# Performance work log

Measured on AMD Instinct MI355X. Metric: run time of the kernel, lower is better.

The kernel has to match this reference:

```python
import jax, jax.numpy as jnp
import numpy as np

N_NODES = 50000
N_EDGES = 800000
NFEAT, NHID, NCLASS = 512, 256, 128
N_UV = 2048


def gcn_layer(x, adj_row, adj_col, adj_val, W, b):
    # support = x @ W ; out = A @ support (sparse COO spmm) + b
    support = x @ W                                   # [N, out]
    msgs = adj_val[:, None] * support[adj_col]        # [E, out]
    out = jax.ops.segment_sum(msgs, adj_row, num_segments=N_NODES)
    return out + b


def setup_inputs() -> dict:
    key = jax.random.key(0)
    ks = jax.random.split(key, 12)
    u = jax.random.randint(ks[0], (N_UV,), 0, N_NODES)
    v = jax.random.randint(ks[1], (N_UV,), 0, N_NODES)
    x = jax.random.normal(ks[2], (N_NODES, NFEAT), dtype=jnp.float32)
    adj_row = jnp.sort(jax.random.randint(ks[3], (N_EDGES,), 0, N_NODES))
    adj_col = jax.random.randint(ks[4], (N_EDGES,), 0, N_NODES)
    adj_val = jax.random.uniform(ks[5], (N_EDGES,), dtype=jnp.float32)
    s1 = 1.0 / np.sqrt(NHID)
    s2 = 1.0 / np.sqrt(NCLASS)
    W1 = jax.random.uniform(ks[6], (NFEAT, NHID), minval=-s1, maxval=s1, dtype=jnp.float32)
    b1 = jax.random.uniform(ks[7], (NHID,), minval=-s1, maxval=s1, dtype=jnp.float32)
    W2 = jax.random.uniform(ks[8], (NHID, NCLASS), minval=-s2, maxval=s2, dtype=jnp.float32)
    b2 = jax.random.uniform(ks[9], (NCLASS,), minval=-s2, maxval=s2, dtype=jnp.float32)
    We = jax.random.normal(ks[10], (NCLASS, NCLASS), dtype=jnp.float32) * (1.0 / np.sqrt(NCLASS))
    return {"u": u, "v": v, "x": x, "adj_row": adj_row, "adj_col": adj_col,
            "adj_val": adj_val, "W1": W1, "b1": b1, "W2": W2, "b2": b2, "We": We}


def reference(u, v, x, adj_row, adj_col, adj_val, W1, b1, W2, b2, We):
    # layer 1: GCN + ReLU (dropout is identity in eval mode)
    h = jax.nn.relu(gcn_layer(x, adj_row, adj_col, adj_val, W1, b1))
    # layer 2: GCN
    z = gcn_layer(h, adj_row, adj_col, adj_val, W2, b2)          # [N, nclass]
    # edge scoring: sigmoid(w_edge(z[u]) @ z[v].T)
    zu = z[u] @ We.T                                             # [U, nclass] (nn.Linear: x @ W.T)
    zv = z[v]                                                    # [V, nclass]
    p_uv = jax.nn.sigmoid(zu @ zv.T)                             # [U, V]
    return p_uv
```

## Files before the change

### kernel.cpp

```cpp
#include <hip/hip_runtime.h>
#include <hip/hip_bf16.h>
#include <math.h>

#define N_NODES 50000
#define N_EDGES 800000
#define NFEAT   512
#define NHID    256
#define NCLASS  128
#define N_UV    2048

#define Q24_SCALE  524288.0f
#define Q24_INV    1.9073486328125e-6f

typedef __bf16    bf16x8 __attribute__((ext_vector_type(8)));
typedef short     s16x8  __attribute__((ext_vector_type(8)));
typedef float     f32x4  __attribute__((ext_vector_type(4)));

struct __attribute__((packed)) U3 { unsigned a, b, c; };

__device__ __forceinline__ unsigned short bf16_rn(float f) {
  unsigned u = __float_as_uint(f);
  u += 0x7fffu + ((u >> 16) & 1u);
  return (unsigned short)(u >> 16);
}
__device__ __forceinline__ float bf16_to_f(unsigned short h) {
  return __uint_as_float(((unsigned)h) << 16);
}
__device__ __forceinline__ void unpack24(unsigned a, unsigned b, unsigned c,
                                         int& e0, int& e1, int& e2, int& e3) {
  e0 = ((int)(a << 8)) >> 8;
  e1 = ((int)((b << 16) | ((a >> 24) << 8))) >> 8;
  e2 = ((int)((c << 24) | ((b >> 16) << 8))) >> 8;
  e3 = ((int)c) >> 8;
}

#define LDSPAD 72

template <bool ASPLIT, bool BSPLIT, int OMODE>
__global__ __launch_bounds__(256, 2) void gemm_mfma_split(
    const float* __restrict__ Af,
    const unsigned short* __restrict__ Ahi, const unsigned short* __restrict__ Alo,
    const float* __restrict__ BTf,
    const unsigned short* __restrict__ BThi, const unsigned short* __restrict__ BTlo,
    float* __restrict__ C, unsigned char* __restrict__ Cq, int M, int N, int K) {
  __shared__ unsigned short sAh[128 * LDSPAD];
  __shared__ unsigned short sAl[128 * LDSPAD];
  __shared__ unsigned short sBh[128 * LDSPAD];
  __shared__ unsigned short sBl[128 * LDSPAD];

  const int tid  = threadIdx.x;
  const int lane = tid & 63;
  const int wave = tid >> 6;
  const int wm   = (wave >> 1) << 6;
  const int wn   = (wave & 1) << 6;
  const int lm   = lane & 15;
  const int quad = lane >> 4;
  const int m0   = blockIdx.y * 128;
  const int n0   = blockIdx.x * 128;

  const int r32 = tid >> 4;
  const int c32 = (tid & 15) * 4;
  const int r16 = tid >> 3;
  const int c16 = (tid & 7) * 8;

  float4 pA[8]; s16x8 pAh[4], pAl[4];
  float4 pB[8]; s16x8 pBh[4], pBl[4];

  f32x4 acc[4][4];
#pragma unroll
  for (int i = 0; i < 4; ++i)
#pragma unroll
    for (int j = 0; j < 4; ++j)
#pragma unroll
      for (int r = 0; r < 4; ++r) acc[i][j][r] = 0.f;

#define LOAD_TILE(k0)                                                          \
  do {                                                                         \
    if (ASPLIT) {                                                              \
      _Pragma("unroll") for (int p = 0; p < 8; ++p) {                          \
        const int m = m0 + p * 16 + r32;                                       \
        pA[p] = make_float4(0.f, 0.f, 0.f, 0.f);                               \
        if (m < M) pA[p] = *(const float4*)&Af[(size_t)m * K + (k0) + c32];    \
      }                                                                        \
    } else {                                                                   \
      _Pragma("unroll") for (int p = 0; p < 4; ++p) {                          \
        const int m = m0 + p * 32 + r16;                                       \
        _Pragma("unroll") for (int e = 0; e < 8; ++e) { pAh[p][e] = 0; pAl[p][e] = 0; } \
        if (m < M) {                                                           \
          pAh[p] = *(const s16x8*)&Ahi[(size_t)m * K + (k0) + c16];            \
          pAl[p] = *(const s16x8*)&Alo[(size_t)m * K + (k0) + c16];            \
        }                                                                      \
      }                                                                        \
    }                                                                          \
    if (BSPLIT) {                                                              \
      _Pragma("unroll") for (int p = 0; p < 8; ++p) {                          \
        const int n = n0 + p * 16 + r32;                                       \
        pB[p] = *(const float4*)&BTf[(size_t)n * K + (k0) + c32];              \
      }                                                                        \
    } else {                                                                   \
      _Pragma("unroll") for (int p = 0; p < 4; ++p) {                          \
        pBh[p] = *(const s16x8*)&BThi[(size_t)(n0 + p * 32 + r16) * K + (k0) + c16]; \
        pBl[p] = *(const s16x8*)&BTlo[(size_t)(n0 + p * 32 + r16) * K + (k0) + c16]; \
      }                                                                        \
    }                                                                          \
  } while (0)

#define SPLIT4(v, hv, lv)                                                      \
  hv.x = bf16_rn(v.x); lv.x = bf16_rn(v.x - bf16_to_f(hv.x));                  \
  hv.y = bf16_rn(v.y); lv.y = bf16_rn(v.y - bf16_to_f(hv.y));                  \
  hv.z = bf16_rn(v.z); lv.z = bf16_rn(v.z - bf16_to_f(hv.z));                  \
  hv.w = bf16_rn(v.w); lv.w = bf16_rn(v.w - bf16_to_f(hv.w));

#define STORE_TILE()                                                           \
  do {                                                                         \
    if (ASPLIT) {                                                              \
      _Pragma("unroll") for (int p = 0; p < 8; ++p) {                          \
        ushort4 hv, lv; SPLIT4(pA[p], hv, lv);                                 \
        const int row = p * 16 + r32;                                          \
        *(ushort4*)&sAh[row * LDSPAD + c32] = hv;                              \
        *(ushort4*)&sAl[row * LDSPAD + c32] = lv;                              \
      }                                                                        \
    } else {                                                                   \
      _Pragma("unroll") for (int p = 0; p < 4; ++p) {                          \
        const int row = p * 32 + r16;                                          \
        *(s16x8*)&sAh[row * LDSPAD + c16] = pAh[p];                            \
        *(s16x8*)&sAl[row * LDSPAD + c16] = pAl[p];                            \
      }                                                                        \
    }                                                                          \
    if (BSPLIT) {                                                              \
      _Pragma("unroll") for (int p = 0; p < 8; ++p) {                          \
        ushort4 hv, lv; SPLIT4(pB[p], hv, lv);                                 \
        const int row = p * 16 + r32;                                          \
        *(ushort4*)&sBh[row * LDSPAD + c32] = hv;                              \
        *(ushort4*)&sBl[row * LDSPAD + c32] = lv;                              \
      }                                                                        \
    } else {                                                                   \
      _Pragma("unroll") for (int p = 0; p < 4; ++p) {                          \
        const int row = p * 32 + r16;                                          \
        *(s16x8*)&sBh[row * LDSPAD + c16] = pBh[p];                            \
        *(s16x8*)&sBl[row * LDSPAD + c16] = pBl[p];                            \
      }                                                                        \
    }                                                                          \
  } while (0)

  LOAD_TILE(0);

  for (int k0 = 0; k0 < K; k0 += 64) {
    if (k0) __syncthreads();
    STORE_TILE();
    __syncthreads();
    if (k0 + 64 < K) LOAD_TILE(k0 + 64);

#pragma unroll
    for (int ks = 0; ks < 2; ++ks) {
      const int koff = ks * 32 + quad * 8;
      bf16x8 aH[4], aL[4], bH[4], bL[4];
#pragma unroll
      for (int i = 0; i < 4; ++i) {
        const int r = wm + i * 16 + lm;
        aH[i] = __builtin_bit_cast(bf16x8, *(const s16x8*)&sAh[r * LDSPAD + koff]);
        aL[i] = __builtin_bit_cast(bf16x8, *(const s16x8*)&sAl[r * LDSPAD + koff]);
      }
#pragma unroll
      for (int j = 0; j < 4; ++j) {
        const int r = wn + j * 16 + lm;
        bH[j] = __builtin_bit_cast(bf16x8, *(const s16x8*)&sBh[r * LDSPAD + koff]);
        bL[j] = __builtin_bit_cast(bf16x8, *(const s16x8*)&sBl[r * LDSPAD + koff]);
      }
#pragma unroll
      for (int i = 0; i < 4; ++i)
#pragma unroll
        for (int j = 0; j < 4; ++j) {
          acc[i][j] = __builtin_amdgcn_mfma_f32_16x16x32_bf16(aH[i], bH[j], acc[i][j], 0, 0, 0);
          acc[i][j] = __builtin_amdgcn_mfma_f32_16x16x32_bf16(aH[i], bL[j], acc[i][j], 0, 0, 0);
          acc[i][j] = __builtin_amdgcn_mfma_f32_16x16x32_bf16(aL[i], bH[j], acc[i][j], 0, 0, 0);
        }
    }
  }

#pragma unroll
  for (int i = 0; i < 4; ++i)
#pragma unroll
    for (int j = 0; j < 4; ++j) {
      const int col = n0 + wn + j * 16 + lm;
#pragma unroll
      for (int r = 0; r < 4; ++r) {
        const int row = m0 + wm + i * 16 + quad * 4 + r;
        if (row < M) {
          float v = acc[i][j][r];
          if (OMODE == 1) {
            v = 1.f / (1.f + expf(-v));
            C[(size_t)row * N + col] = v;
          } else if (OMODE == 2) {
            int q = __float2int_rn(v * Q24_SCALE);
            q = q > 8388607 ? 8388607 : (q < -8388608 ? -8388608 : q);
            unsigned char* p = Cq + ((size_t)row * N + col) * 3;
            p[0] = (unsigned char)(q & 0xFF);
            p[1] = (unsigned char)((q >> 8) & 0xFF);
            p[2] = (unsigned char)((q >> 16) & 0xFF);
          } else {
            C[(size_t)row * N + col] = v;
          }
        }
      }
    }
#undef LOAD_TILE
#undef STORE_TILE
#undef SPLIT4
}

__global__ __launch_bounds__(256) void prep_all(
    const int* __restrict__ rows, int* __restrict__ row_ptr,
    const float* __restrict__ W1, unsigned short* __restrict__ W1Thi,
    unsigned short* __restrict__ W1Tlo,
    const float* __restrict__ W2, unsigned short* __restrict__ W2Thi,
    unsigned short* __restrict__ W2Tlo) {
  const int idx = blockIdx.x * 256 + threadIdx.x;
  if (idx < N_EDGES) {
    const int r = rows[idx];
    const int rprev = (idx == 0) ? -1 : rows[idx - 1];
    for (int n = rprev + 1; n <= r; ++n) row_ptr[n] = idx;
    if (idx == N_EDGES - 1)
      for (int n = r + 1; n <= N_NODES; ++n) row_ptr[n] = N_EDGES;
  }
  if (idx < NFEAT * NHID) {
    const int n = idx / NFEAT;
    const int k = idx - n * NFEAT;
    const float f = W1[(size_t)k * NHID + n];
    const unsigned short h = bf16_rn(f);
    W1Thi[idx] = h;
    W1Tlo[idx] = bf16_rn(f - bf16_to_f(h));
  }
  if (idx < NHID * NCLASS) {
    const int n = idx / NHID;
    const int k = idx - n * NHID;
    const float f = W2[(size_t)k * NCLASS + n];
    const unsigned short h = bf16_rn(f);
    W2Thi[idx] = h;
    W2Tlo[idx] = bf16_rn(f - bf16_to_f(h));
  }
}

__global__ __launch_bounds__(256, 4) void spmm256_q24_split(
    const unsigned char* __restrict__ Sq, const int* __restrict__ row_ptr,
    const int* __restrict__ cols, const float* __restrict__ vals,
    const float4* __restrict__ bias4,
    unsigned short* __restrict__ outHi, unsigned short* __restrict__ outLo) {
  const int wave = threadIdx.x >> 6;
  const int lane = threadIdx.x & 63;
  const int node = blockIdx.x * 4 + wave;

  const int lou = __builtin_amdgcn_readfirstlane(row_ptr[node]);
  const int hiu = __builtin_amdgcn_readfirstlane(row_ptr[node + 1]);

  float4 acc = make_float4(0.f, 0.f, 0.f, 0.f);
  const int lane12 = lane * 12;

  for (int base = lou; base < hiu; base += 16) {
    int   c[16];
    float w[16];
    if (base + 16 <= hiu) {
#pragma unroll
      for (int t = 0; t < 16; ++t) {
        c[t] = cols[base + t];
        w[t] = vals[base + t] * Q24_INV;
      }
    } else {
#pragma unroll
      for (int t = 0; t < 16; ++t) {
        const int idx = base + t;
        const int ide = idx < hiu ? idx : hiu - 1;
        c[t] = cols[ide];
        w[t] = idx < hiu ? vals[ide] * Q24_INV : 0.f;
      }
    }
    U3 d[16];
#pragma unroll
    for (int t = 0; t < 16; ++t)
      d[t] = *(const U3*)&Sq[(size_t)c[t] * (NHID * 3) + lane12];
#pragma unroll
    for (int t = 0; t < 16; ++t) {
      int e0, e1, e2, e3;
      unpack24(d[t].a, d[t].b, d[t].c, e0, e1, e2, e3);
      acc.x = fmaf(w[t], (float)e0, acc.x);
      acc.y = fmaf(w[t], (float)e1, acc.y);
      acc.z = fmaf(w[t], (float)e2, acc.z);
      acc.w = fmaf(w[t], (float)e3, acc.w);
    }
  }

  const float4 b = bias4[lane];
  acc.x = fmaxf(acc.x + b.x, 0.f);
  acc.y = fmaxf(acc.y + b.y, 0.f);
  acc.z = fmaxf(acc.z + b.z, 0.f);
  acc.w = fmaxf(acc.w + b.w, 0.f);

  ushort4 hv, lv;
  hv.x = bf16_rn(acc.x); lv.x = bf16_rn(acc.x - bf16_to_f(hv.x));
  hv.y = bf16_rn(acc.y); lv.y = bf16_rn(acc.y - bf16_to_f(hv.y));
  hv.z = bf16_rn(acc.z); lv.z = bf16_rn(acc.z - bf16_to_f(hv.z));
  hv.w = bf16_rn(acc.w); lv.w = bf16_rn(acc.w - bf16_to_f(hv.w));
  const size_t o = (size_t)node * NHID + lane * 4;
  *(ushort4*)&outHi[o] = hv;
  *(ushort4*)&outLo[o] = lv;
}

__global__ __launch_bounds__(256) void spmm128_f32_list(
    const float4* __restrict__ S4, const int* __restrict__ row_ptr,
    const int* __restrict__ cols, const float* __restrict__ vals,
    const float4* __restrict__ bias4,
    const int* __restrict__ u, const int* __restrict__ v,
    float4* __restrict__ out4) {
  const int wave = threadIdx.x >> 6;
  const int lane = threadIdx.x & 63;
  const int half = lane >> 5;
  const int l32  = lane & 31;
  const int idx  = blockIdx.x * 4 + wave;
  const int node = idx < N_UV ? u[idx] : v[idx - N_UV];

  const int lo = row_ptr[node];
  const int hi = row_ptr[node + 1];

  float4 acc = make_float4(0.f, 0.f, 0.f, 0.f);
  int e = lo + half;
  for (; e + 6 < hi; e += 8) {
    int c[4]; float w[4];
#pragma unroll
    for (int t = 0; t < 4; ++t) { c[t] = cols[e + 2 * t]; w[t] = vals[e + 2 * t]; }
    float4 r[4];
#pragma unroll
    for (int t = 0; t < 4; ++t) r[t] = S4[(size_t)c[t] * 32 + l32];
#pragma unroll
    for (int t = 0; t < 4; ++t) {
      acc.x = fmaf(w[t], r[t].x, acc.x); acc.y = fmaf(w[t], r[t].y, acc.y);
      acc.z = fmaf(w[t], r[t].z, acc.z); acc.w = fmaf(w[t], r[t].w, acc.w);
    }
  }
  for (; e < hi; e += 2) {
    const int c = cols[e];
    const float w = vals[e];
    const float4 r = S4[(size_t)c * 32 + l32];
    acc.x = fmaf(w, r.x, acc.x); acc.y = fmaf(w, r.y, acc.y);
    acc.z = fmaf(w, r.z, acc.z); acc.w = fmaf(w, r.w, acc.w);
  }

  acc.x += __shfl_xor(acc.x, 32);
  acc.y += __shfl_xor(acc.y, 32);
  acc.z += __shfl_xor(acc.z, 32);
  acc.w += __shfl_xor(acc.w, 32);

  if (half == 0) {
    const float4 b = bias4[l32];
    acc.x += b.x; acc.y += b.y; acc.z += b.z; acc.w += b.w;
    out4[(size_t)idx * 32 + l32] = acc;
  }
}

extern "C" void kernel_launch(void* const* d_in, const int* in_sizes, int n_in,
                              void* d_out, int out_size, void* d_ws, size_t ws_size,
                              hipStream_t stream) {
  const int*   u       = (const int*)  d_in[0];
  const int*   v       = (const int*)  d_in[1];
  const float* x       = (const float*)d_in[2];
  const int*   adj_row = (const int*)  d_in[3];
  const int*   adj_col = (const int*)  d_in[4];
  const float* adj_val = (const float*)d_in[5];
  const float* W1      = (const float*)d_in[6];
  const float* b1      = (const float*)d_in[7];
  const float* W2      = (const float*)d_in[8];
  const float* b2      = (const float*)d_in[9];
  const float* We      = (const float*)d_in[10];
  float* out = (float*)d_out;

  char* wsb = (char*)d_ws;
  unsigned char* S1q = (unsigned char*)wsb;
  float* S2  = (float*)wsb;
  float* ZUV = (float*)(wsb + (size_t)N_NODES * NCLASS * sizeof(float));
  char* rB = wsb + (size_t)N_NODES * NHID * sizeof(float);
  unsigned short* Hhi = (unsigned short*)rB;
  unsigned short* Hlo = Hhi + (size_t)N_NODES * NHID;
  float* ZU = (float*)rB;
  unsigned short* W1Thi = (unsigned short*)out;
  unsigned short* W1Tlo = W1Thi + NHID * NFEAT;
  unsigned short* W2Thi = W1Tlo + NHID * NFEAT;
  unsigned short* W2Tlo = W2Thi + NCLASS * NHID;
  int* row_ptr = (int*)(W2Tlo + NCLASS * NHID);

  prep_all<<<(N_EDGES + 255) / 256, 256, 0, stream>>>(
      adj_row, row_ptr, W1, W1Thi, W1Tlo, W2, W2Thi, W2Tlo);

  gemm_mfma_split<true, false, 2>
      <<<dim3(NHID / 128, (N_NODES + 127) / 128), 256, 0, stream>>>(
      x, nullptr, nullptr, nullptr, W1Thi, W1Tlo,
      nullptr, S1q, N_NODES, NHID, NFEAT);

  spmm256_q24_split<<<N_NODES / 4, 256, 0, stream>>>(
      S1q, row_ptr, adj_col, adj_val, (const float4*)b1, Hhi, Hlo);

  gemm_mfma_split<false, false, 0>
      <<<dim3(NCLASS / 128, (N_NODES + 127) / 128), 256, 0, stream>>>(
      nullptr, Hhi, Hlo, nullptr, W2Thi, W2Tlo,
      S2, nullptr, N_NODES, NCLASS, NHID);

  spmm128_f32_list<<<(2 * N_UV) / 4, 256, 0, stream>>>(
      (const float4*)S2, row_ptr, adj_col, adj_val, (const float4*)b2,
      u, v, (float4*)ZUV);

  gemm_mfma_split<true, true, 0>
      <<<dim3(NCLASS / 128, N_UV / 128), 256, 0, stream>>>(
      ZUV, nullptr, nullptr, We, nullptr, nullptr,
      ZU, nullptr, N_UV, NCLASS, NCLASS);

  gemm_mfma_split<true, true, 1>
      <<<dim3(N_UV / 128, N_UV / 128), 256, 0, stream>>>(
      ZU, nullptr, nullptr, ZUV + (size_t)N_UV * NCLASS, nullptr, nullptr,
      out, nullptr, N_UV, N_UV, NCLASS);
}
```

Before: 356.0 us.

## Add 512-thread GEMM that reads pre-split B fragments directly from global

```diff
diff --git a/kernel.cpp b/kernel.cpp
--- a/kernel.cpp
+++ b/kernel.cpp
@@ -36,13 +36,154 @@
 
 #define LDSPAD 72
 
-template <bool ASPLIT, bool BSPLIT, int OMODE>
-__global__ __launch_bounds__(256, 2) void gemm_mfma_split(
+template <bool ASPLIT, int OMODE>
+__global__ __launch_bounds__(512, 4) void gemm_mfma_wide(
     const float* __restrict__ Af,
     const unsigned short* __restrict__ Ahi, const unsigned short* __restrict__ Alo,
-    const float* __restrict__ BTf,
     const unsigned short* __restrict__ BThi, const unsigned short* __restrict__ BTlo,
     float* __restrict__ C, unsigned char* __restrict__ Cq, int M, int N, int K) {
+  __shared__ unsigned short sAh[128 * LDSPAD];
+  __shared__ unsigned short sAl[128 * LDSPAD];
+
+  const int tid  = threadIdx.x;
+  const int lane = tid & 63;
+  const int wave = tid >> 6;
+  const int wm   = (wave >> 2) << 6;
+  const int wn   = (wave & 3) << 5;
+  const int lm   = lane & 15;
+  const int quad = lane >> 4;
+  const int m0   = blockIdx.y * 128;
+  const int n0   = blockIdx.x * 128;
+
+  const int r32 = tid >> 4;
+  const int c32 = (tid & 15) * 4;
+  const int r16 = tid >> 3;
+  const int c16 = (tid & 7) * 8;
+
+  float4 pA[4]; s16x8 pAh[2], pAl[2];
+
+  f32x4 acc[4][2];
+#pragma unroll
+  for (int i = 0; i < 4; ++i)
+#pragma unroll
+    for (int j = 0; j < 2; ++j)
+#pragma unroll
+      for (int r = 0; r < 4; ++r) acc[i][j][r] = 0.f;
+
+#define LOAD_TILE(k0)                                                          \
+  do {                                                                         \
+    if (ASPLIT) {                                                              \
+      _Pragma("unroll") for (int p = 0; p < 4; ++p) {                          \
+        const int m = m0 + p * 32 + r32;                                       \
+        pA[p] = make_float4(0.f, 0.f, 0.f, 0.f);                               \
+        if (m < M) pA[p] = *(const float4*)&Af[(size_t)m * K + (k0) + c32];    \
+      }                                                                        \
+    } else {                                                                   \
+      _Pragma("unroll") for (int p = 0; p < 2; ++p) {                          \
+        const int m = m0 + p * 64 + r16;                                       \
+        _Pragma("unroll") for (int e = 0; e < 8; ++e) { pAh[p][e] = 0; pAl[p][e] = 0; } \
+        if (m < M) {                                                           \
+          pAh[p] = *(const s16x8*)&Ahi[(size_t)m * K + (k0) + c16];            \
+          pAl[p] = *(const s16x8*)&Alo[(size_t)m * K + (k0) + c16];            \
+        }                                                                      \
+      }                                                                        \
+    }                                                                          \
+  } while (0)
+
+#define SPLIT4W(v, hv, lv)                                                     \
+  hv.x = bf16_rn(v.x); lv.x = bf16_rn(v.x - bf16_to_f(hv.x));                  \
+  hv.y = bf16_rn(v.y); lv.y = bf16_rn(v.y - bf16_to_f(hv.y));                  \
+  hv.z = bf16_rn(v.z); lv.z = bf16_rn(v.z - bf16_to_f(hv.z));                  \
+  hv.w = bf16_rn(v.w); lv.w = bf16_rn(v.w - bf16_to_f(hv.w));
+
+#define STORE_TILE()                                                           \
+  do {                                                                         \
+    if (ASPLIT) {                                                              \
+      _Pragma("unroll") for (int p = 0; p < 4; ++p) {                          \
+        ushort4 hv, lv; SPLIT4W(pA[p], hv, lv);                                \
+        const int row = p * 32 + r32;                                          \
+        *(ushort4*)&sAh[row * LDSPAD + c32] = hv;                              \
+        *(ushort4*)&sAl[row * LDSPAD + c32] = lv;                              \
+      }                                                                        \
+    } else {                                                                   \
+      _Pragma("unroll") for (int p = 0; p < 2; ++p) {                          \
+        const int row = p * 64 + r16;                                          \
+        *(s16x8*)&sAh[row * LDSPAD + c16] = pAh[p];                            \
+        *(s16x8*)&sAl[row * LDSPAD + c16] = pAl[p];                            \
+      }                                                                        \
+    }                                                                          \
+  } while (0)
+
+  LOAD_TILE(0);
+
+  const unsigned short* Bhrow = BThi + (size_t)(n0 + wn + lm) * K;
+  const unsigned short* Blrow = BTlo + (size_t)(n0 + wn + lm) * K;
+
+  for (int k0 = 0; k0 < K; k0 += 64) {
+    if (k0) __syncthreads();
+    STORE_TILE();
+    __syncthreads();
+    if (k0 + 64 < K) LOAD_TILE(k0 + 64);
+
+#pragma unroll
+    for (int ks = 0; ks < 2; ++ks) {
+      const int koff = ks * 32 + quad * 8;
+      bf16x8 aH[4], aL[4], bH[2], bL[2];
+#pragma unroll
+      for (int i = 0; i < 4; ++i) {
+        const int r = wm + i * 16 + lm;
+        aH[i] = __builtin_bit_cast(bf16x8, *(const s16x8*)&sAh[r * LDSPAD + koff]);
+        aL[i] = __builtin_bit_cast(bf16x8, *(const s16x8*)&sAl[r * LDSPAD + koff]);
+      }
+#pragma unroll
+      for (int j = 0; j < 2; ++j) {
+        const size_t off = (size_t)(j * 16) * K + k0 + koff;
+        bH[j] = __builtin_bit_cast(bf16x8, *(const s16x8*)(Bhrow + off));
+        bL[j] = __builtin_bit_cast(bf16x8, *(const s16x8*)(Blrow + off));
+      }
+#pragma unroll
+      for (int i = 0; i < 4; ++i)
+#pragma unroll
+        for (int j = 0; j < 2; ++j) {
+          acc[i][j] = __builtin_amdgcn_mfma_f32_16x16x32_bf16(aH[i], bH[j], acc[i][j], 0, 0, 0);
+          acc[i][j] = __builtin_amdgcn_mfma_f32_16x16x32_bf16(aH[i], bL[j], acc[i][j], 0, 0, 0);
+          acc[i][j] = __builtin_amdgcn_mfma_f32_16x16x32_bf16(aL[i], bH[j], acc[i][j], 0, 0, 0);
+        }
+    }
+  }
+
+#pragma unroll
+  for (int i = 0; i < 4; ++i)
+#pragma unroll
+    for (int j = 0; j < 2; ++j) {
+      const int col = n0 + wn + j * 16 + lm;
+#pragma unroll
+      for (int r = 0; r < 4; ++r) {
+        const int row = m0 + wm + i * 16 + quad * 4 + r;
+        if (row < M) {
+          float v = acc[i][j][r];
+          if (OMODE == 2) {
+            int q = __float2int_rn(v * Q24_SCALE);
+            q = q > 8388607 ? 8388607 : (q < -8388608 ? -8388608 : q);
+            unsigned char* p = Cq + ((size_t)row * N + col) * 3;
+            p[0] = (unsigned char)(q & 0xFF);
+            p[1] = (unsigned char)((q >> 8) & 0xFF);
+            p[2] = (unsigned char)((q >> 16) & 0xFF);
+          } else {
+            C[(size_t)row * N + col] = v;
+          }
+        }
+      }
+    }
+#undef LOAD_TILE
+#undef STORE_TILE
+#undef SPLIT4W
+}
+
+template <int OMODE>
+__global__ __launch_bounds__(256, 2) void gemm_mfma_split(
+    const float* __restrict__ Af, const float* __restrict__ BTf,
+    float* __restrict__ C, int M, int N, int K) {
   __shared__ unsigned short sAh[128 * LDSPAD];
   __shared__ unsigned short sAl[128 * LDSPAD];
   __shared__ unsigned short sBh[128 * LDSPAD];
@@ -60,11 +201,9 @@
 
   const int r32 = tid >> 4;
   const int c32 = (tid & 15) * 4;
-  const int r16 = tid >> 3;
-  const int c16 = (tid & 7) * 8;
-
-  float4 pA[8]; s16x8 pAh[4], pAl[4];
-  float4 pB[8]; s16x8 pBh[4], pBl[4];
+
+  float4 pA[8];
+  float4 pB[8];
 
   f32x4 acc[4][4];
 #pragma unroll
@@ -76,32 +215,14 @@
 
 #define LOAD_TILE(k0)                                                          \
   do {                                                                         \
-    if (ASPLIT) {                                                              \
-      _Pragma("unroll") for (int p = 0; p < 8; ++p) {                          \
-        const int m = m0 + p * 16 + r32;                                       \
-        pA[p] = make_float4(0.f, 0.f, 0.f, 0.f);                               \
-        if (m < M) pA[p] = *(const float4*)&Af[(size_t)m * K + (k0) + c32];    \
-      }                                                                        \
-    } else {                                                                   \
-      _Pragma("unroll") for (int p = 0; p < 4; ++p) {                          \
-        const int m = m0 + p * 32 + r16;                                       \
-        _Pragma("unroll") for (int e = 0; e < 8; ++e) { pAh[p][e] = 0; pAl[p][e] = 0; } \
-        if (m < M) {                                                           \
-          pAh[p] = *(const s16x8*)&Ahi[(size_t)m * K + (k0) + c16];            \
-          pAl[p] = *(const s16x8*)&Alo[(size_t)m * K + (k0) + c16];            \
-        }                                                                      \
-      }                                                                        \
+    _Pragma("unroll") for (int p = 0; p < 8; ++p) {                            \
+      const int m = m0 + p * 16 + r32;                                         \
+      pA[p] = make_float4(0.f, 0.f, 0.f, 0.f);                                 \
+      if (m < M) pA[p] = *(const float4*)&Af[(size_t)m * K + (k0) + c32];      \
     }                                                                          \
-    if (BSPLIT) {                                                              \
-      _Pragma("unroll") for (int p = 0; p < 8; ++p) {                          \
-        const int n = n0 + p * 16 + r32;                                       \
-        pB[p] = *(const float4*)&BTf[(size_t)n * K + (k0) + c32];              \
-      }                                                                        \
-    } else {                                                                   \
-      _Pragma("unroll") for (int p = 0; p < 4; ++p) {                          \
-        pBh[p] = *(const s16x8*)&BThi[(size_t)(n0 + p * 32 + r16) * K + (k0) + c16]; \
-        pBl[p] = *(const s16x8*)&BTlo[(size_t)(n0 + p * 32 + r16) * K + (k0) + c16]; \
-      }                                                                        \
+    _Pragma("unroll") for (int p = 0; p < 8; ++p) {                            \
+      const int n = n0 + p * 16 + r32;                                         \
+      pB[p] = *(const float4*)&BTf[(size_t)n * K + (k0) + c32];                \
     }                                                                          \
   } while (0)
 
@@ -113,33 +234,17 @@
 
 #define STORE_TILE()                                                           \
   do {                                                                         \
-    if (ASPLIT) {                                                              \
-      _Pragma("unroll") for (int p = 0; p < 8; ++p) {                          \
-        ushort4 hv, lv; SPLIT4(pA[p], hv, lv);                                 \
-        const int row = p * 16 + r32;                                          \
-        *(ushort4*)&sAh[row * LDSPAD + c32] = hv;                              \
-        *(ushort4*)&sAl[row * LDSPAD + c32] = lv;                              \
-      }                                                                        \
-    } else {                                                                   \
-      _Pragma("unroll") for (int p = 0; p < 4; ++p) {                          \
-        const int row = p * 32 + r16;                                          \
-        *(s16x8*)&sAh[row * LDSPAD + c16] = pAh[p];                            \
-        *(s16x8*)&sAl[row * LDSPAD + c16] = pAl[p];                            \
-      }                                                                        \
+    _Pragma("unroll") for (int p = 0; p < 8; ++p) {                            \
+      ushort4 hv, lv; SPLIT4(pA[p], hv, lv);                                   \
+      const int row = p * 16 + r32;                                            \
+      *(ushort4*)&sAh[row * LDSPAD + c32] = hv;                                \
+      *(ushort4*)&sAl[row * LDSPAD + c32] = lv;                                \
     }                                                                          \
-    if (BSPLIT) {                                                              \
-      _Pragma("unroll") for (int p = 0; p < 8; ++p) {                          \
-        ushort4 hv, lv; SPLIT4(pB[p], hv, lv);                                 \
-        const int row = p * 16 + r32;                                          \
-        *(ushort4*)&sBh[row * LDSPAD + c32] = hv;                              \
-        *(ushort4*)&sBl[row * LDSPAD + c32] = lv;                              \
-      }                                                                        \
-    } else {                                                                   \
-      _Pragma("unroll") for (int p = 0; p < 4; ++p) {                          \
-        const int row = p * 32 + r16;                                          \
-        *(s16x8*)&sBh[row * LDSPAD + c16] = pBh[p];                            \
-        *(s16x8*)&sBl[row * LDSPAD + c16] = pBl[p];                            \
-      }                                                                        \
+    _Pragma("unroll") for (int p = 0; p < 8; ++p) {                            \
+      ushort4 hv, lv; SPLIT4(pB[p], hv, lv);                                   \
+      const int row = p * 16 + r32;                                            \
+      *(ushort4*)&sBh[row * LDSPAD + c32] = hv;                                \
+      *(ushort4*)&sBl[row * LDSPAD + c32] = lv;                                \
     }                                                                          \
   } while (0)
 
@@ -188,19 +293,8 @@
         const int row = m0 + wm + i * 16 + quad * 4 + r;
         if (row < M) {
           float v = acc[i][j][r];
-          if (OMODE == 1) {
-            v = 1.f / (1.f + expf(-v));
-            C[(size_t)row * N + col] = v;
-          } else if (OMODE == 2) {
-            int q = __float2int_rn(v * Q24_SCALE);
-            q = q > 8388607 ? 8388607 : (q < -8388608 ? -8388608 : q);
-            unsigned char* p = Cq + ((size_t)row * N + col) * 3;
-            p[0] = (unsigned char)(q & 0xFF);
-            p[1] = (unsigned char)((q >> 8) & 0xFF);
-            p[2] = (unsigned char)((q >> 16) & 0xFF);
-          } else {
-            C[(size_t)row * N + col] = v;
-          }
+          if (OMODE == 1) v = 1.f / (1.f + expf(-v));
+          C[(size_t)row * N + col] = v;
         }
       }
     }
@@ -389,30 +483,28 @@
   prep_all<<<(N_EDGES + 255) / 256, 256, 0, stream>>>(
       adj_row, row_ptr, W1, W1Thi, W1Tlo, W2, W2Thi, W2Tlo);
 
-  gemm_mfma_split<true, false, 2>
-      <<<dim3(NHID / 128, (N_NODES + 127) / 128), 256, 0, stream>>>(
-      x, nullptr, nullptr, nullptr, W1Thi, W1Tlo,
+  gemm_mfma_wide<true, 2>
+      <<<dim3(NHID / 128, (N_NODES + 127) / 128), 512, 0, stream>>>(
+      x, nullptr, nullptr, W1Thi, W1Tlo,
       nullptr, S1q, N_NODES, NHID, NFEAT);
 
   spmm256_q24_split<<<N_NODES / 4, 256, 0, stream>>>(
       S1q, row_ptr, adj_col, adj_val, (const float4*)b1, Hhi, Hlo);
 
-  gemm_mfma_split<false, false, 0>
-      <<<dim3(NCLASS / 128, (N_NODES + 127) / 128), 256, 0, stream>>>(
-      nullptr, Hhi, Hlo, nullptr, W2Thi, W2Tlo,
+  gemm_mfma_wide<false, 0>
+      <<<dim3(NCLASS / 128, (N_NODES + 127) / 128), 512, 0, stream>>>(
+      nullptr, Hhi, Hlo, W2Thi, W2Tlo,
       S2, nullptr, N_NODES, NCLASS, NHID);
 
   spmm128_f32_list<<<(2 * N_UV) / 4, 256, 0, stream>>>(
       (const float4*)S2, row_ptr, adj_col, adj_val, (const float4*)b2,
       u, v, (float4*)ZUV);
 
-  gemm_mfma_split<true, true, 0>
+  gemm_mfma_split<0>
       <<<dim3(NCLASS / 128, N_UV / 128), 256, 0, stream>>>(
-      ZUV, nullptr, nullptr, We, nullptr, nullptr,
-      ZU, nullptr, N_UV, NCLASS, NCLASS);
-
-  gemm_mfma_split<true, true, 1>
+      ZUV, We, ZU, N_UV, NCLASS, NCLASS);
+
+  gemm_mfma_split<1>
       <<<dim3(N_UV / 128, N_UV / 128), 256, 0, stream>>>(
-      ZU, nullptr, nullptr, ZUV + (size_t)N_UV * NCLASS, nullptr, nullptr,
-      out, nullptr, N_UV, N_UV, NCLASS);
-}
+      ZU, ZUV + (size_t)N_UV * NCLASS, out, N_UV, N_UV, NCLASS);
+}
```

Measured after the change: 395.3 us. +11.0%, slower.
